# Kernel tuning notes

Hardware: AMD Instinct MI355X
Metric: run time of the kernel (lower is better)

Reference implementation:

```python
import jax, jax.numpy as jnp
import numpy as np

EMBED_DIM = 1024
NUM_HEADS = 16
HEAD_DIM = EMBED_DIM // NUM_HEADS


def layer_norm(x, gamma, beta, eps=1e-5):
    mu = jnp.mean(x, axis=-1, keepdims=True)
    var = jnp.var(x, axis=-1, keepdims=True)
    return (x - mu) * jax.lax.rsqrt(var + eps) * gamma + beta


def setup_inputs() -> dict:
    key = jax.random.key(0)
    ks = jax.random.split(key, 8)
    D = EMBED_DIM
    s = 1.0 / np.sqrt(D)
    x = jax.random.normal(ks[0], (2, 2048, D), dtype=jnp.float32)
    Wq = jax.random.uniform(ks[1], (D, D), jnp.float32, -s, s)
    Wk = jax.random.uniform(ks[2], (D, D), jnp.float32, -s, s)
    Wv = jax.random.uniform(ks[3], (D, D), jnp.float32, -s, s)
    W1 = jax.random.uniform(ks[4], (D, 4 * D), jnp.float32, -s, s)
    b1 = jnp.zeros((4 * D,), jnp.float32)
    W2 = jax.random.uniform(ks[5], (4 * D, D), jnp.float32, -1.0 / np.sqrt(4 * D), 1.0 / np.sqrt(4 * D))
    b2 = jnp.zeros((D,), jnp.float32)
    g1 = jnp.ones((D,), jnp.float32); be1 = jnp.zeros((D,), jnp.float32)
    g2 = jnp.ones((D,), jnp.float32); be2 = jnp.zeros((D,), jnp.float32)
    return {"x": x, "Wq": Wq, "Wk": Wk, "Wv": Wv, "W1": W1, "b1": b1,
            "W2": W2, "b2": b2, "g1": g1, "be1": be1, "g2": g2, "be2": be2}


def reference(x, Wq, Wk, Wv, W1, b1, W2, b2, g1, be1, g2, be2):
    B, S, D = x.shape
    H, Hd = NUM_HEADS, HEAD_DIM
    x_norm = layer_norm(x, g1, be1)
    # QKV projections (no bias), split into heads: [B, H, S, Hd]
    q = (x_norm @ Wq).reshape(B, S, H, Hd).transpose(0, 2, 1, 3)
    k = (x_norm @ Wk).reshape(B, S, H, Hd).transpose(0, 2, 1, 3)
    v = (x_norm @ Wv).reshape(B, S, H, Hd).transpose(0, 2, 1, 3)
    energy = jnp.einsum('bhqd,bhkd->bhqk', q, k)
    attn = jax.nn.softmax(energy / jnp.sqrt(jnp.float32(Hd)), axis=-1)
    out = jnp.einsum('bhqk,bhkd->bhqd', attn, v)
    attention = out.transpose(0, 2, 1, 3).reshape(B, S, D)
    x_res = attention + x
    x_norm2 = layer_norm(x_res, g2, be2)
    # Faithful quirk: FFN applied to x_res (not x_norm2)
    ffn_out = jax.nn.relu(x_res @ W1 + b1) @ W2 + b2
    return ffn_out + x_norm2
```

## Files before the change

### kernel.cpp

```cpp
#include <hip/hip_runtime.h>
#include <hip/hip_bf16.h>
#include <stdint.h>

typedef __hip_bfloat16 bf16;
typedef __attribute__((ext_vector_type(4))) float f32x4;
typedef __attribute__((ext_vector_type(8))) short s16x8;
typedef __attribute__((ext_vector_type(4))) short s16x4;

#define DEV static __device__ __forceinline__

DEV short f2bf(float f) {
  bf16 h = __float2bfloat16(f);
  short s;
  __builtin_memcpy(&s, &h, 2);
  return s;
}
DEV float bf2f(short s) {
  bf16 h;
  __builtin_memcpy(&h, &s, 2);
  return __bfloat162float(h);
}

__global__ __launch_bounds__(256) void transpose_cvt(
    const float* __restrict__ W, bf16* __restrict__ Wt, int K, int N)
{
  __shared__ float tile[32][33];
  const int n0 = blockIdx.x << 5;
  const int k0 = blockIdx.y << 5;
  const int tx = threadIdx.x & 31, ty = threadIdx.x >> 5;
#pragma unroll
  for (int i = 0; i < 4; ++i)
    tile[ty + i * 8][tx] = W[(size_t)(k0 + ty + i * 8) * N + n0 + tx];
  __syncthreads();
#pragma unroll
  for (int i = 0; i < 4; ++i)
    Wt[(size_t)(n0 + ty + i * 8) * K + k0 + tx] = __float2bfloat16(tile[tx][ty + i * 8]);
}

__global__ __launch_bounds__(256) void ln_bf16(
    const float* __restrict__ x, const float* __restrict__ g,
    const float* __restrict__ be, bf16* __restrict__ out)
{
  const int t = threadIdx.x;
  const size_t row = blockIdx.x;
  const float4 v = ((const float4*)(x + row * 1024))[t];
  float s = v.x + v.y + v.z + v.w;
  float ss = v.x * v.x + v.y * v.y + v.z * v.z + v.w * v.w;
#pragma unroll
  for (int off = 32; off > 0; off >>= 1) {
    s += __shfl_down(s, off);
    ss += __shfl_down(ss, off);
  }
  __shared__ float sh[8];
  const int wave = t >> 6, lane = t & 63;
  if (!lane) { sh[wave] = s; sh[4 + wave] = ss; }
  __syncthreads();
  s = sh[0] + sh[1] + sh[2] + sh[3];
  ss = sh[4] + sh[5] + sh[6] + sh[7];
  const float mean = s * (1.f / 1024.f);
  const float rstd = rsqrtf(ss * (1.f / 1024.f) - mean * mean + 1e-5f);
  const float4 gv = ((const float4*)g)[t];
  const float4 bv = ((const float4*)be)[t];
  s16x4 o;
  o[0] = f2bf((v.x - mean) * rstd * gv.x + bv.x);
  o[1] = f2bf((v.y - mean) * rstd * gv.y + bv.y);
  o[2] = f2bf((v.z - mean) * rstd * gv.z + bv.z);
  o[3] = f2bf((v.w - mean) * rstd * gv.w + bv.w);
  ((s16x4*)(out + row * 1024))[t] = o;
}

__global__ __launch_bounds__(256) void add_ln_bf16(
    const float* __restrict__ a, const float* __restrict__ x,
    const float* __restrict__ g, const float* __restrict__ be,
    bf16* __restrict__ xres, bf16* __restrict__ xnorm)
{
  const int t = threadIdx.x;
  const size_t row = blockIdx.x;
  const float4 av = ((const float4*)(a + row * 1024))[t];
  const float4 xv = ((const float4*)(x + row * 1024))[t];
  float4 v;
  v.x = av.x + xv.x; v.y = av.y + xv.y; v.z = av.z + xv.z; v.w = av.w + xv.w;
  float s = v.x + v.y + v.z + v.w;
  float ss = v.x * v.x + v.y * v.y + v.z * v.z + v.w * v.w;
#pragma unroll
  for (int off = 32; off > 0; off >>= 1) {
    s += __shfl_down(s, off);
    ss += __shfl_down(ss, off);
  }
  __shared__ float sh[8];
  const int wave = t >> 6, lane = t & 63;
  if (!lane) { sh[wave] = s; sh[4 + wave] = ss; }
  __syncthreads();
  s = sh[0] + sh[1] + sh[2] + sh[3];
  ss = sh[4] + sh[5] + sh[6] + sh[7];
  const float mean = s * (1.f / 1024.f);
  const float rstd = rsqrtf(ss * (1.f / 1024.f) - mean * mean + 1e-5f);
  const float4 gv = ((const float4*)g)[t];
  const float4 bv = ((const float4*)be)[t];
  s16x4 r, o;
  r[0] = f2bf(v.x); r[1] = f2bf(v.y); r[2] = f2bf(v.z); r[3] = f2bf(v.w);
  o[0] = f2bf((v.x - mean) * rstd * gv.x + bv.x);
  o[1] = f2bf((v.y - mean) * rstd * gv.y + bv.y);
  o[2] = f2bf((v.z - mean) * rstd * gv.z + bv.z);
  o[3] = f2bf((v.w - mean) * rstd * gv.w + bv.w);
  ((s16x4*)(xres + row * 1024))[t] = r;
  ((s16x4*)(xnorm + row * 1024))[t] = o;
}

template <int EPI>
__global__ __launch_bounds__(256) void gemm_bt(
    const bf16* __restrict__ A, const bf16* __restrict__ Bt,
    void* __restrict__ C, const float* __restrict__ bias,
    const bf16* __restrict__ add_bf16, int M, int N, int K)
{
  __shared__ bf16 sA0[128 * 64];
  __shared__ bf16 sB0[128 * 64];
  __shared__ bf16 sA1[128 * 64];
  __shared__ bf16 sB1[128 * 64];
  const int tid = threadIdx.x;
  const int wave = tid >> 6, lane = tid & 63;
  const int fr = lane & 15, fg = lane >> 4;
  const int f7 = fr & 7;
  const int wr = wave >> 1, wc = wave & 1;
  const int nbx = N >> 7;
  int bid = blockIdx.x;
  if ((gridDim.x & 7) == 0) {
    const int cpx = gridDim.x >> 3;
    bid = (bid & 7) * cpx + (bid >> 3);
  }
  const int brow = (bid / nbx) << 7;
  const int bcol = (bid % nbx) << 7;

  f32x4 acc[4][4] = {};

  const int rsub = lane >> 3;
  const int cl = (lane & 7) ^ rsub;
  size_t ga[4], gb[4];
  int la[4];
#pragma unroll
  for (int j = 0; j < 4; ++j) {
    const int r = wave * 32 + j * 8;
    ga[j] = (size_t)(brow + r + rsub) * K + cl * 8;
    gb[j] = (size_t)(bcol + r + rsub) * K + cl * 8;
    la[j] = r * 64;
  }

#define GSTAGE(SA, SB, koff)                                                   \
  do {                                                                         \
    _Pragma("unroll")                                                          \
    for (int jj = 0; jj < 4; ++jj) {                                           \
      __builtin_amdgcn_global_load_lds(                                        \
          (const __attribute__((address_space(1))) uint32_t*)(A + ga[jj] + (koff)), \
          (__attribute__((address_space(3))) uint32_t*)(&SA[la[jj]]), 16, 0, 0);  \
      __builtin_amdgcn_global_load_lds(                                        \
          (const __attribute__((address_space(1))) uint32_t*)(Bt + gb[jj] + (koff)),\
          (__attribute__((address_space(3))) uint32_t*)(&SB[la[jj]]), 16, 0, 0);  \
    }                                                                          \
  } while (0)

#define COMPUTE(SA, SB)                                                        \
  do {                                                                         \
    s16x8 af[4][2], bfr[4][2];                                                 \
    _Pragma("unroll")                                                          \
    for (int m = 0; m < 4; ++m)                                                \
      _Pragma("unroll")                                                        \
      for (int kk = 0; kk < 2; ++kk)                                           \
        af[m][kk] = *(const s16x8*)(&SA[(wr * 64 + m * 16 + fr) * 64 +         \
                                        (((kk * 4 + fg) ^ f7) << 3)]);         \
    _Pragma("unroll")                                                          \
    for (int n = 0; n < 4; ++n)                                                \
      _Pragma("unroll")                                                        \
      for (int kk = 0; kk < 2; ++kk)                                           \
        bfr[n][kk] = *(const s16x8*)(&SB[(wc * 64 + n * 16 + fr) * 64 +        \
                                         (((kk * 4 + fg) ^ f7) << 3)]);        \
    _Pragma("unroll")                                                          \
    for (int kk = 0; kk < 2; ++kk)                                             \
      _Pragma("unroll")                                                        \
      for (int m = 0; m < 4; ++m)                                              \
        _Pragma("unroll")                                                      \
        for (int n = 0; n < 4; ++n)                                            \
          acc[m][n] = __builtin_amdgcn_mfma_f32_16x16x32_bf16(                 \
              af[m][kk], bfr[n][kk], acc[m][n], 0, 0, 0);                      \
  } while (0)

  GSTAGE(sA0, sB0, 0);
  __syncthreads();

  int kt = 0;
  for (;;) {
    if (kt + 64 < K) {
      GSTAGE(sA1, sB1, kt + 64);
      COMPUTE(sA0, sB0);
      __syncthreads();
    } else {
      COMPUTE(sA0, sB0);
      break;
    }
    kt += 64;
    if (kt + 64 < K) {
      GSTAGE(sA0, sB0, kt + 64);
      COMPUTE(sA1, sB1);
      __syncthreads();
    } else {
      COMPUTE(sA1, sB1);
      break;
    }
    kt += 64;
  }
#undef GSTAGE
#undef COMPUTE

  const int crow = brow + wr * 64;
  const int ccol = bcol + wc * 64;
#pragma unroll
  for (int m = 0; m < 4; ++m) {
#pragma unroll
    for (int n = 0; n < 4; ++n) {
      const int col = ccol + n * 16 + fr;
#pragma unroll
      for (int j = 0; j < 4; ++j) {
        const int row = crow + m * 16 + fg * 4 + j;
        float v = acc[m][n][j];
        if (EPI == 0) {
          ((bf16*)C)[(size_t)row * N + col] = __float2bfloat16(v);
        } else if (EPI == 1) {
          v += bias[col];
          v = fmaxf(v, 0.f);
          ((bf16*)C)[(size_t)row * N + col] = __float2bfloat16(v);
        } else {
          float a;
          {
            bf16 hb = add_bf16[(size_t)row * N + col];
            a = __bfloat162float(hb);
          }
          ((float*)C)[(size_t)row * N + col] = v + bias[col] + a;
        }
      }
    }
  }
}

template <int EPI>
__global__ __launch_bounds__(512) void gemm256_bt(
    const bf16* __restrict__ A, const bf16* __restrict__ Bt,
    void* __restrict__ C, const float* __restrict__ bias, int M, int N, int K)
{
  __shared__ bf16 sA0[256 * 64];
  __shared__ bf16 sB0[256 * 64];
  __shared__ bf16 sA1[256 * 64];
  __shared__ bf16 sB1[256 * 64];
  const int tid = threadIdx.x;
  const int wave = tid >> 6, lane = tid & 63;
  const int fr = lane & 15, fg = lane >> 4;
  const int f7 = fr & 7;
  const int wr = wave >> 2, wc = wave & 3;
  const int nbx = N >> 8;
  int bid = blockIdx.x;
  if ((gridDim.x & 7) == 0) {
    const int cpx = gridDim.x >> 3;
    bid = (bid & 7) * cpx + (bid >> 3);
  }
  const int brow = (bid / nbx) << 8;
  const int bcol = (bid % nbx) << 8;

  f32x4 acc[8][4] = {};

  const int rsub = lane >> 3;
  const int cl = (lane & 7) ^ rsub;
  size_t ga[4], gb[4];
  int la[4];
#pragma unroll
  for (int j = 0; j < 4; ++j) {
    const int r = j * 64 + wave * 8;
    ga[j] = (size_t)(brow + r + rsub) * K + cl * 8;
    gb[j] = (size_t)(bcol + r + rsub) * K + cl * 8;
    la[j] = r * 64;
  }

#define STG6(SA, SB, koff)                                                     \
  do {                                                                         \
    _Pragma("unroll")                                                          \
    for (int jj = 0; jj < 4; ++jj) {                                           \
      __builtin_amdgcn_global_load_lds(                                        \
          (const __attribute__((address_space(1))) uint32_t*)(A + ga[jj] + (koff)), \
          (__attribute__((address_space(3))) uint32_t*)(&SA[la[jj]]), 16, 0, 0);  \
      __builtin_amdgcn_global_load_lds(                                        \
          (const __attribute__((address_space(1))) uint32_t*)(Bt + gb[jj] + (koff)),\
          (__attribute__((address_space(3))) uint32_t*)(&SB[la[jj]]), 16, 0, 0);  \
    }                                                                          \
  } while (0)

#define CMP6(SA, SB)                                                           \
  do {                                                                         \
    s16x8 bfr[4][2];                                                           \
    _Pragma("unroll")                                                          \
    for (int n = 0; n < 4; ++n)                                                \
      _Pragma("unroll")                                                        \
      for (int kk = 0; kk < 2; ++kk)                                           \
        bfr[n][kk] = *(const s16x8*)(&SB[(wc * 64 + n * 16 + fr) * 64 +        \
                                         (((kk * 4 + fg) ^ f7) << 3)]);        \
    __builtin_amdgcn_s_setprio(1);                                             \
    _Pragma("unroll")                                                          \
    for (int m = 0; m < 8; ++m) {                                              \
      s16x8 afm[2];                                                            \
      _Pragma("unroll")                                                        \
      for (int kk = 0; kk < 2; ++kk)                                           \
        afm[kk] = *(const s16x8*)(&SA[(wr * 128 + m * 16 + fr) * 64 +          \
                                      (((kk * 4 + fg) ^ f7) << 3)]);           \
      _Pragma("unroll")                                                        \
      for (int kk = 0; kk < 2; ++kk)                                           \
        _Pragma("unroll")                                                      \
        for (int n = 0; n < 4; ++n)                                            \
          acc[m][n] = __builtin_amdgcn_mfma_f32_16x16x32_bf16(                 \
              afm[kk], bfr[n][kk], acc[m][n], 0, 0, 0);                        \
    }                                                                          \
    __builtin_amdgcn_s_setprio(0);                                             \
  } while (0)

  STG6(sA0, sB0, 0);

  int kt = 0;
  for (;;) {
    if (kt + 64 < K) {
      STG6(sA1, sB1, kt + 64);
      asm volatile("s_waitcnt vmcnt(8)" ::: "memory");
    } else {
      asm volatile("s_waitcnt vmcnt(0)" ::: "memory");
    }
    __builtin_amdgcn_s_barrier();
    __builtin_amdgcn_sched_barrier(0);
    CMP6(sA0, sB0);
    if (kt + 64 >= K) break;
    __builtin_amdgcn_s_barrier();
    __builtin_amdgcn_sched_barrier(0);
    kt += 64;
    if (kt + 64 < K) {
      STG6(sA0, sB0, kt + 64);
      asm volatile("s_waitcnt vmcnt(8)" ::: "memory");
    } else {
      asm volatile("s_waitcnt vmcnt(0)" ::: "memory");
    }
    __builtin_amdgcn_s_barrier();
    __builtin_amdgcn_sched_barrier(0);
    CMP6(sA1, sB1);
    if (kt + 64 >= K) break;
    __builtin_amdgcn_s_barrier();
    __builtin_amdgcn_sched_barrier(0);
    kt += 64;
  }
#undef STG6
#undef CMP6

  const int crow = brow + wr * 128;
  const int ccol = bcol + wc * 64;
#pragma unroll
  for (int m = 0; m < 8; ++m) {
#pragma unroll
    for (int n = 0; n < 4; ++n) {
      const int col = ccol + n * 16 + fr;
#pragma unroll
      for (int j = 0; j < 4; ++j) {
        const int row = crow + m * 16 + fg * 4 + j;
        float v = acc[m][n][j];
        if (EPI == 0) {
          ((bf16*)C)[(size_t)row * N + col] = __float2bfloat16(v);
        } else {
          v += bias[col];
          v = fmaxf(v, 0.f);
          ((bf16*)C)[(size_t)row * N + col] = __float2bfloat16(v);
        }
      }
    }
  }
}

__global__ __launch_bounds__(512, 4) void attn_fwd(
    const bf16* __restrict__ QK, const bf16* __restrict__ Vt,
    float* __restrict__ Out)
{
  const int LDK = 2048;
  const int qt = blockIdx.x;
  const int bh = blockIdx.y;
  const int b = bh >> 4, h = bh & 15;
  const int tid = threadIdx.x;
  const int wave = tid >> 6, lane = tid & 63;
  const int fr = lane & 15, fg = lane >> 4;
  const int f7 = fr & 7;

  const short* base = (const short*)QK + (size_t)b * 2048 * LDK;
  const short* Qp = base + h * 64;
  const short* Kp = base + 1024 + h * 64;
  const short* Vp = (const short*)Vt + (size_t)h * 64 * 4096 + b * 2048;
  const int q0 = qt * 128 + wave * 16;

  __shared__ short Kbuf[2][64 * 64];
  __shared__ short Vbuf[2][64 * 64];
  __shared__ short P_lds[8][16 * 72];
  short* Pw = P_lds[wave];

  const int rsub = lane >> 3;
  const int clog = (lane & 7) ^ rsub;
  const short* Ksrc = Kp + (size_t)(8 * wave + rsub) * LDK + clog * 8;
  const short* Vsrc = Vp + (size_t)(8 * wave + rsub) * 4096 + clog * 8;

  s16x8 qf0 = *(const s16x8*)(Qp + (size_t)(q0 + fr) * LDK + fg * 8);
  s16x8 qf1 = *(const s16x8*)(Qp + (size_t)(q0 + fr) * LDK + 32 + fg * 8);
#pragma unroll
  for (int i = 0; i < 8; ++i) {
    qf0[i] = f2bf(bf2f(qf0[i]) * 0.125f);
    qf1[i] = f2bf(bf2f(qf1[i]) * 0.125f);
  }

  f32x4 acc[4] = {};
  f32x4 mrow = {-1e30f, -1e30f, -1e30f, -1e30f};
  f32x4 lrow = {};

#define STAGE(bi, koff)                                                        \
  do {                                                                         \
    __builtin_amdgcn_global_load_lds(                                          \
        (const __attribute__((address_space(1))) uint32_t*)(Ksrc + (size_t)(koff) * LDK), \
        (__attribute__((address_space(3))) uint32_t*)(&Kbuf[bi][wave * 512]),  \
        16, 0, 0);                                                             \
    __builtin_amdgcn_global_load_lds(                                          \
        (const __attribute__((address_space(1))) uint32_t*)(Vsrc + (koff)),    \
        (__attribute__((address_space(3))) uint32_t*)(&Vbuf[bi][wave * 512]),  \
        16, 0, 0);                                                             \
  } while (0)

  int cur = 0;
  STAGE(0, 0);

  for (int kt = 0; kt < 2048; kt += 64) {
    if (kt + 64 < 2048) {
      STAGE(cur ^ 1, kt + 64);
      asm volatile("s_waitcnt vmcnt(2)" ::: "memory");
    } else {
      asm volatile("s_waitcnt vmcnt(0)" ::: "memory");
    }
    __builtin_amdgcn_s_barrier();
    __builtin_amdgcn_sched_barrier(0);

    const short* Kb = Kbuf[cur];
    const short* Vb = Vbuf[cur];

    f32x4 e[4];
    __builtin_amdgcn_s_setprio(1);
#pragma unroll
    for (int t = 0; t < 4; ++t) {
      const int ro = (t * 16 + fr) * 64;
      const s16x8 k0 = *(const s16x8*)(Kb + ro + ((fg ^ f7) << 3));
      const s16x8 k1 = *(const s16x8*)(Kb + ro + (((4 + fg) ^ f7) << 3));
      f32x4 z = {};
      z = __builtin_amdgcn_mfma_f32_16x16x32_bf16(qf0, k0, z, 0, 0, 0);
      z = __builtin_amdgcn_mfma_f32_16x16x32_bf16(qf1, k1, z, 0, 0, 0);
      e[t] = z;
    }
    __builtin_amdgcn_s_setprio(0);

    f32x4 lmx;
#pragma unroll
    for (int j = 0; j < 4; ++j)
      lmx[j] = fmaxf(fmaxf(e[0][j], e[1][j]), fmaxf(e[2][j], e[3][j]));
    const bool need = (lmx[0] > mrow[0] + 8.f) | (lmx[1] > mrow[1] + 8.f) |
                      (lmx[2] > mrow[2] + 8.f) | (lmx[3] > mrow[3] + 8.f);
    if (__any(need)) {
      f32x4 mx = lmx;
#pragma unroll
      for (int d = 1; d < 16; d <<= 1)
#pragma unroll
        for (int j = 0; j < 4; ++j) mx[j] = fmaxf(mx[j], __shfl_xor(mx[j], d));
#pragma unroll
      for (int j = 0; j < 4; ++j) {
        const float mn = fmaxf(mrow[j], mx[j]);
        const float al = __expf(mrow[j] - mn);
        lrow[j] *= al;
        mrow[j] = mn;
#pragma unroll
        for (int nn = 0; nn < 4; ++nn) acc[nn][j] *= al;
      }
    }

#pragma unroll
    for (int j = 0; j < 4; ++j) {
#pragma unroll
      for (int t = 0; t < 4; ++t) e[t][j] = __expf(e[t][j] - mrow[j]);
      lrow[j] += (e[0][j] + e[1][j]) + (e[2][j] + e[3][j]);
    }

#pragma unroll
    for (int t = 0; t < 4; ++t)
#pragma unroll
      for (int j = 0; j < 4; ++j)
        Pw[(fg * 4 + j) * 72 + t * 16 + fr] = f2bf(e[t][j]);
    const s16x8 pf0 = *(const s16x8*)(Pw + fr * 72 + fg * 8);
    const s16x8 pf1 = *(const s16x8*)(Pw + fr * 72 + 32 + fg * 8);

    __builtin_amdgcn_s_setprio(1);
#pragma unroll
    for (int nn = 0; nn < 4; ++nn) {
      const int ro = (nn * 16 + fr) * 64;
      const s16x8 vf0 = *(const s16x8*)(Vb + ro + ((fg ^ f7) << 3));
      const s16x8 vf1 = *(const s16x8*)(Vb + ro + (((4 + fg) ^ f7) << 3));
      acc[nn] = __builtin_amdgcn_mfma_f32_16x16x32_bf16(pf0, vf0, acc[nn], 0, 0, 0);
      acc[nn] = __builtin_amdgcn_mfma_f32_16x16x32_bf16(pf1, vf1, acc[nn], 0, 0, 0);
    }
    __builtin_amdgcn_s_setprio(0);

    __builtin_amdgcn_s_barrier();
    __builtin_amdgcn_sched_barrier(0);
    cur ^= 1;
  }
#undef STAGE

#pragma unroll
  for (int d = 1; d < 16; d <<= 1)
#pragma unroll
    for (int j = 0; j < 4; ++j) lrow[j] += __shfl_xor(lrow[j], d);
  f32x4 inv;
#pragma unroll
  for (int j = 0; j < 4; ++j) inv[j] = 1.0f / lrow[j];
  float* outp = Out + (size_t)(b * 2048 + q0) * 1024 + h * 64;
#pragma unroll
  for (int nn = 0; nn < 4; ++nn)
#pragma unroll
    for (int j = 0; j < 4; ++j)
      outp[(size_t)(fg * 4 + j) * 1024 + nn * 16 + fr] = acc[nn][j] * inv[j];
}

extern "C" void kernel_launch(void* const* d_in, const int* in_sizes, int n_in,
                              void* d_out, int out_size, void* d_ws, size_t ws_size,
                              hipStream_t stream)
{
  const float* x   = (const float*)d_in[0];
  const float* Wq  = (const float*)d_in[1];
  const float* Wk  = (const float*)d_in[2];
  const float* Wv  = (const float*)d_in[3];
  const float* W1  = (const float*)d_in[4];
  const float* b1  = (const float*)d_in[5];
  const float* W2  = (const float*)d_in[6];
  const float* b2  = (const float*)d_in[7];
  const float* g1  = (const float*)d_in[8];
  const float* be1 = (const float*)d_in[9];
  const float* g2  = (const float*)d_in[10];
  const float* be2 = (const float*)d_in[11];
  float* out = (float*)d_out;

  const int M = 4096, D = 1024, DF = 4096;

  bf16* Wqk_t = (bf16*)d_ws;
  bf16* Wv_t  = Wqk_t + (size_t)2048 * 1024;
  bf16* W1t   = Wv_t + (size_t)1024 * 1024;
  bf16* W2t   = W1t + (size_t)4096 * 1024;
  bf16* big   = W2t + (size_t)4096 * 1024;
  bf16* QK    = big;
  bf16* Vt    = big + (size_t)8 * 1024 * 1024;
  bf16* hbuf  = big;
  char* p2    = (char*)(big + (size_t)16 * 1024 * 1024);
  bf16* xnorm = (bf16*)p2;
  float* attnO = (float*)p2;
  char* p3    = p2 + (size_t)M * D * sizeof(float);
  bf16* xres  = (bf16*)p3;
  bf16* xnorm2 = xres + (size_t)M * D;

  transpose_cvt<<<dim3(32, 32), 256, 0, stream>>>(Wq, Wqk_t, D, D);
  transpose_cvt<<<dim3(32, 32), 256, 0, stream>>>(Wk, Wqk_t + (size_t)D * D, D, D);
  transpose_cvt<<<dim3(32, 32), 256, 0, stream>>>(Wv, Wv_t, D, D);
  transpose_cvt<<<dim3(128, 32), 256, 0, stream>>>(W1, W1t, D, DF);
  transpose_cvt<<<dim3(32, 128), 256, 0, stream>>>(W2, W2t, DF, D);
  ln_bf16<<<M, 256, 0, stream>>>(x, g1, be1, xnorm);
  gemm_bt<0><<<(M / 128) * (2048 / 128), 256, 0, stream>>>(
      xnorm, Wqk_t, QK, nullptr, nullptr, M, 2048, D);
  gemm_bt<0><<<(D / 128) * (M / 128), 256, 0, stream>>>(
      Wv_t, xnorm, Vt, nullptr, nullptr, D, M, D);
  attn_fwd<<<dim3(16, 32), 512, 0, stream>>>(QK, Vt, attnO);
  add_ln_bf16<<<M, 256, 0, stream>>>(attnO, x, g2, be2, xres, xnorm2);
  gemm256_bt<1><<<(M / 256) * (DF / 256), 512, 0, stream>>>(
      xres, W1t, hbuf, b1, M, DF, D);
  gemm_bt<2><<<(M / 128) * (D / 128), 256, 0, stream>>>(
      hbuf, W2t, out, b2, xnorm2, M, D, DF);
}
```

Measured before the change: 237.9 us.

## Pipeline GEMM with vmcnt waits, use exp2 and MFMA row sums in attention

```diff
diff --git a/kernel.cpp b/kernel.cpp
--- a/kernel.cpp
+++ b/kernel.cpp
@@ -173,6 +173,7 @@
       for (int kk = 0; kk < 2; ++kk)                                           \
         bfr[n][kk] = *(const s16x8*)(&SB[(wc * 64 + n * 16 + fr) * 64 +        \
                                          (((kk * 4 + fg) ^ f7) << 3)]);        \
+    __builtin_amdgcn_s_setprio(1);                                             \
     _Pragma("unroll")                                                          \
     for (int kk = 0; kk < 2; ++kk)                                             \
       _Pragma("unroll")                                                        \
@@ -181,30 +182,38 @@
         for (int n = 0; n < 4; ++n)                                            \
           acc[m][n] = __builtin_amdgcn_mfma_f32_16x16x32_bf16(                 \
               af[m][kk], bfr[n][kk], acc[m][n], 0, 0, 0);                      \
+    __builtin_amdgcn_s_setprio(0);                                             \
   } while (0)
 
   GSTAGE(sA0, sB0, 0);
-  __syncthreads();
 
   int kt = 0;
   for (;;) {
     if (kt + 64 < K) {
       GSTAGE(sA1, sB1, kt + 64);
-      COMPUTE(sA0, sB0);
-      __syncthreads();
+      asm volatile("s_waitcnt vmcnt(8)" ::: "memory");
     } else {
-      COMPUTE(sA0, sB0);
-      break;
-    }
+      asm volatile("s_waitcnt vmcnt(0)" ::: "memory");
+    }
+    __builtin_amdgcn_s_barrier();
+    __builtin_amdgcn_sched_barrier(0);
+    COMPUTE(sA0, sB0);
+    if (kt + 64 >= K) break;
+    __builtin_amdgcn_s_barrier();
+    __builtin_amdgcn_sched_barrier(0);
     kt += 64;
     if (kt + 64 < K) {
       GSTAGE(sA0, sB0, kt + 64);
-      COMPUTE(sA1, sB1);
-      __syncthreads();
+      asm volatile("s_waitcnt vmcnt(8)" ::: "memory");
     } else {
-      COMPUTE(sA1, sB1);
-      break;
-    }
+      asm volatile("s_waitcnt vmcnt(0)" ::: "memory");
+    }
+    __builtin_amdgcn_s_barrier();
+    __builtin_amdgcn_sched_barrier(0);
+    COMPUTE(sA1, sB1);
+    if (kt + 64 >= K) break;
+    __builtin_amdgcn_s_barrier();
+    __builtin_amdgcn_sched_barrier(0);
     kt += 64;
   }
 #undef GSTAGE
@@ -395,7 +404,7 @@
 
   __shared__ short Kbuf[2][64 * 64];
   __shared__ short Vbuf[2][64 * 64];
-  __shared__ short P_lds[8][16 * 72];
+  __shared__ short P_lds[8][16 * 80];
   short* Pw = P_lds[wave];
 
   const int rsub = lane >> 3;
@@ -403,17 +412,24 @@
   const short* Ksrc = Kp + (size_t)(8 * wave + rsub) * LDK + clog * 8;
   const short* Vsrc = Vp + (size_t)(8 * wave + rsub) * 4096 + clog * 8;
 
+  const float QS = 0.125f * 1.44269504f;
   s16x8 qf0 = *(const s16x8*)(Qp + (size_t)(q0 + fr) * LDK + fg * 8);
   s16x8 qf1 = *(const s16x8*)(Qp + (size_t)(q0 + fr) * LDK + 32 + fg * 8);
 #pragma unroll
   for (int i = 0; i < 8; ++i) {
-    qf0[i] = f2bf(bf2f(qf0[i]) * 0.125f);
-    qf1[i] = f2bf(bf2f(qf1[i]) * 0.125f);
-  }
+    qf0[i] = f2bf(bf2f(qf0[i]) * QS);
+    qf1[i] = f2bf(bf2f(qf1[i]) * QS);
+  }
+
+  s16x8 ones;
+#pragma unroll
+  for (int i = 0; i < 8; ++i) ones[i] = (short)0x3F80;
 
   f32x4 acc[4] = {};
+  f32x4 lacc = {};
   f32x4 mrow = {-1e30f, -1e30f, -1e30f, -1e30f};
-  f32x4 lrow = {};
+
+  const int prow = (fr & 3) * 4 + (fr >> 2);
 
 #define STAGE(bi, koff)                                                        \
   do {                                                                         \
@@ -461,8 +477,8 @@
 #pragma unroll
     for (int j = 0; j < 4; ++j)
       lmx[j] = fmaxf(fmaxf(e[0][j], e[1][j]), fmaxf(e[2][j], e[3][j]));
-    const bool need = (lmx[0] > mrow[0] + 8.f) | (lmx[1] > mrow[1] + 8.f) |
-                      (lmx[2] > mrow[2] + 8.f) | (lmx[3] > mrow[3] + 8.f);
+    const bool need = (lmx[0] > mrow[0] + 11.f) | (lmx[1] > mrow[1] + 11.f) |
+                      (lmx[2] > mrow[2] + 11.f) | (lmx[3] > mrow[3] + 11.f);
     if (__any(need)) {
       f32x4 mx = lmx;
 #pragma unroll
@@ -472,8 +488,8 @@
 #pragma unroll
       for (int j = 0; j < 4; ++j) {
         const float mn = fmaxf(mrow[j], mx[j]);
-        const float al = __expf(mrow[j] - mn);
-        lrow[j] *= al;
+        const float al = exp2f(mrow[j] - mn);
+        lacc[j] *= al;
         mrow[j] = mn;
 #pragma unroll
         for (int nn = 0; nn < 4; ++nn) acc[nn][j] *= al;
@@ -481,21 +497,21 @@
     }
 
 #pragma unroll
-    for (int j = 0; j < 4; ++j) {
-#pragma unroll
-      for (int t = 0; t < 4; ++t) e[t][j] = __expf(e[t][j] - mrow[j]);
-      lrow[j] += (e[0][j] + e[1][j]) + (e[2][j] + e[3][j]);
-    }
+    for (int j = 0; j < 4; ++j)
+#pragma unroll
+      for (int t = 0; t < 4; ++t) e[t][j] = exp2f(e[t][j] - mrow[j]);
 
 #pragma unroll
     for (int t = 0; t < 4; ++t)
 #pragma unroll
       for (int j = 0; j < 4; ++j)
-        Pw[(fg * 4 + j) * 72 + t * 16 + fr] = f2bf(e[t][j]);
-    const s16x8 pf0 = *(const s16x8*)(Pw + fr * 72 + fg * 8);
-    const s16x8 pf1 = *(const s16x8*)(Pw + fr * 72 + 32 + fg * 8);
+        Pw[(j * 4 + fg) * 80 + t * 16 + fr] = f2bf(e[t][j]);
+    const s16x8 pf0 = *(const s16x8*)(Pw + prow * 80 + fg * 8);
+    const s16x8 pf1 = *(const s16x8*)(Pw + prow * 80 + 32 + fg * 8);
 
     __builtin_amdgcn_s_setprio(1);
+    lacc = __builtin_amdgcn_mfma_f32_16x16x32_bf16(pf0, ones, lacc, 0, 0, 0);
+    lacc = __builtin_amdgcn_mfma_f32_16x16x32_bf16(pf1, ones, lacc, 0, 0, 0);
 #pragma unroll
     for (int nn = 0; nn < 4; ++nn) {
       const int ro = (nn * 16 + fr) * 64;
@@ -512,13 +528,9 @@
   }
 #undef STAGE
 
-#pragma unroll
-  for (int d = 1; d < 16; d <<= 1)
-#pragma unroll
-    for (int j = 0; j < 4; ++j) lrow[j] += __shfl_xor(lrow[j], d);
   f32x4 inv;
 #pragma unroll
-  for (int j = 0; j < 4; ++j) inv[j] = 1.0f / lrow[j];
+  for (int j = 0; j < 4; ++j) inv[j] = 1.0f / lacc[j];
   float* outp = Out + (size_t)(b * 2048 + q0) * 1024 + h * 64;
 #pragma unroll
   for (int nn = 0; nn < 4; ++nn)
```

New measurement: 263.6 us. +10.8%, slower.
